# Optimization experiments

Hardware: AMD Instinct MI355X
Metric: run time of the kernel (lower is better)

Reference implementation:

```python
import jax, jax.numpy as jnp
import numpy as np

# ---- Cl(3,0,1) algebra constants (basis blades in bitmask order, bit k = e_k) ----
# metric: e0,e1,e2 square to +1 (p=3), e3 squares to 0 (r=1, the projective/null direction)
_METRIC = [1.0, 1.0, 1.0, 0.0]

def _cayley_table():
    C = np.zeros((16, 16, 16), dtype=np.float32)
    for a in range(16):
        for b in range(16):
            # canonical reordering sign
            s, t = 0, a >> 1
            while t:
                s += bin(t & b).count('1')
                t >>= 1
            val = -1.0 if (s & 1) else 1.0
            for k in range(4):
                if (a >> k) & 1 and (b >> k) & 1:
                    val *= _METRIC[k]
            if val != 0.0:
                C[a, b, a ^ b] += val
    return C

_C = jnp.asarray(_cayley_table())                       # [16,16,16] geometric-product table
_POPC = [bin(i).count('1') for i in range(16)]
_REV = jnp.asarray([(-1.0) ** (g * (g - 1) // 2) for g in _POPC], dtype=jnp.float32)  # reverse signs
_G2 = jnp.asarray([1.0 if g == 2 else 0.0 for g in _POPC], dtype=jnp.float32)         # grade-2 mask
_CENTERS = jnp.arange(10, dtype=jnp.float32)

def _gp(a, b):
    # geometric product for small multivector batches
    return jnp.einsum('...i,...j,ijk->...k', a, b, _C)

def _mv_exp(x, n_terms=16):
    # Taylor-series exponential of a multivector (x is a small [L,16] bivector)
    term = jnp.zeros_like(x).at[..., 0].set(1.0)
    acc = term
    for n in range(1, n_terms):
        term = _gp(term, x) / n
        acc = acc + term
    return acc


def setup_inputs() -> dict:
    key = jax.random.key(0)
    k1, k2, k3, k4 = jax.random.split(key, 4)
    B, N, D, K = 32, 100000, 16, 4
    state = jax.random.normal(k1, (B, N, D), dtype=jnp.float32)
    instruction = jax.random.normal(k2, (B, D), dtype=jnp.float32)
    remap_tables = jnp.eye(10, dtype=jnp.float32)[None].repeat(K, axis=0) \
        + 0.01 * jax.random.normal(k3, (K, 10, 10), dtype=jnp.float32)
    selector_w = jax.random.normal(k4, (K, 2), dtype=jnp.float32) / jnp.sqrt(2.0)
    selector_b = jnp.zeros((K,), dtype=jnp.float32)
    return {"state": state, "instruction": instruction, "remap_tables": remap_tables,
            "selector_w": selector_w, "selector_b": selector_b}


def reference(state, instruction, remap_tables, selector_w, selector_b):
    # ---- PGA motor sandwich product ----
    bv = instruction * _G2                                   # grade-2 projection [L,16]
    M = _mv_exp(-0.5 * bv)                                   # motor [L,16]
    M_rev = M * _REV                                         # reverse(M)
    # Precompute per-row left/right multiplication matrices (avoid [L,N,16,16] outer products)
    Lmat = jnp.einsum('li,ijk->ljk', M, _C)                  # left-mult by M:   x_j -> (M x)_k
    Rmat = jnp.einsum('lj,ijk->lik', M_rev, _C)              # right-mult by ~M: y_i -> (y ~M)_k
    tmp = jnp.einsum('lnj,ljk->lnk', state, Lmat)            # M * state
    spatial = jnp.einsum('lni,lik->lnk', tmp, Rmat)          # (M * state) * ~M   [L,N,16]

    # ---- ColorUnit: soft color remap of grade-0, occupancy into grade-4 ----
    sel_input = jnp.stack([instruction[:, 0], instruction[:, 15]], axis=-1)      # [L,2]
    table_weights = jax.nn.softmax(sel_input @ selector_w.T + selector_b, axis=-1)  # [L,K]
    blended = jnp.einsum('lk,kij->lij', table_weights, remap_tables)             # [L,10,10]
    raw_color = spatial[:, :, 0] * 9.0                                           # [L,N]
    diffs = raw_color[..., None] - _CENTERS                                      # [L,N,10]
    soft_color = jax.nn.softmax(-4.0 * diffs * diffs, axis=-1)                   # [L,N,10]
    remapped = jnp.einsum('lni,lij->lnj', soft_color, blended)                   # [L,N,10]
    new_color = jnp.einsum('lni,i->ln', remapped, _CENTERS) / 9.0
    new_occupancy = 1.0 - remapped[:, :, 0]
    out = spatial.at[:, :, 0].set(new_color).at[:, :, 15].set(new_occupancy)
    return out
```

## Files before the change

kernel.cpp:

```cpp
#include <hip/hip_runtime.h>
#include <math.h>

constexpr int cpopc(int x){ int c=0; while(x){ c += x&1; x >>= 1; } return c; }

constexpr float csign(int a, int b){
    if (a & b & 8) return 0.0f;
    int s = 0;
    for (int t = a >> 1; t; t >>= 1) s += cpopc(t & b);
    return (s & 1) ? -1.0f : 1.0f;
}

__device__ constexpr int EVEN[8] = {0,3,5,6,9,10,12,15};
__device__ constexpr int EIDX[16] = {0,-1,-1,1,-1,2,3,-1,-1,4,5,-1,6,-1,-1,7};
__device__ constexpr float REVE[8] = {1.f,-1.f,-1.f,-1.f,-1.f,-1.f,-1.f,1.f};

#define WS_STRIDE 288

__global__ void setup_kernel(const float* __restrict__ instr,
                             const float* __restrict__ remap,
                             const float* __restrict__ selw,
                             const float* __restrict__ selb,
                             float* __restrict__ ws,
                             int B, int K) {
    const int l = blockIdx.x * blockDim.x + threadIdx.x;
    if (l >= B) return;
    const float* ins = instr + l * 16;

    float bv[8];
    bv[0] = 0.f; bv[7] = 0.f;
    #pragma unroll
    for (int m = 1; m < 7; m++) bv[m] = -0.5f * ins[EVEN[m]];

    float term[8], acc[8];
    #pragma unroll
    for (int m = 0; m < 8; m++){ term[m] = (m==0) ? 1.f : 0.f; acc[m] = term[m]; }
    #pragma unroll
    for (int n = 1; n < 16; n++){
        float nt[8];
        #pragma unroll
        for (int m = 0; m < 8; m++) nt[m] = 0.f;
        #pragma unroll
        for (int ia = 0; ia < 8; ia++){
            #pragma unroll
            for (int ib = 0; ib < 8; ib++){
                const float s = csign(EVEN[ia], EVEN[ib]);
                if (s != 0.f) nt[EIDX[EVEN[ia] ^ EVEN[ib]]] += s * term[ia] * bv[ib];
            }
        }
        const float inv = 1.0f / (float)n;
        #pragma unroll
        for (int m = 0; m < 8; m++){ term[m] = nt[m] * inv; acc[m] += term[m]; }
    }

    float P[64];
    #pragma unroll
    for (int ia = 0; ia < 8; ia++)
        #pragma unroll
        for (int ib = 0; ib < 8; ib++)
            P[ia*8+ib] = acc[ia] * (acc[ib] * REVE[ib]);

    float* o = ws + (size_t)l * WS_STRIDE;
    #pragma unroll
    for (int j = 0; j < 16; j++){
        float Trow[16];
        #pragma unroll
        for (int k = 0; k < 16; k++) Trow[k] = 0.f;
        #pragma unroll
        for (int ia = 0; ia < 8; ia++){
            const int A = EVEN[ia];
            const float sa = csign(A, j);
            if (sa != 0.f){
                #pragma unroll
                for (int ib = 0; ib < 8; ib++){
                    const int Bb = EVEN[ib];
                    const float s = sa * csign(A ^ j, Bb);
                    if (s != 0.f) Trow[j ^ A ^ Bb] += s * P[ia*8+ib];
                }
            }
        }
        #pragma unroll
        for (int k = 0; k < 16; k++) o[j*16 + k] = Trow[k];
    }

    const float s0 = ins[0], s1 = ins[15];
    float w[8];
    float mx = -1e30f;
    for (int k = 0; k < K; k++){
        w[k] = s0 * selw[2*k] + s1 * selw[2*k+1] + selb[k];
        mx = fmaxf(mx, w[k]);
    }
    float Z = 0.f;
    for (int k = 0; k < K; k++){ w[k] = __expf(w[k] - mx); Z += w[k]; }
    const float rZ = 1.f / Z;
    for (int k = 0; k < K; k++) w[k] *= rZ;

    for (int i = 0; i < 10; i++){
        float a1 = 0.f, a2 = 0.f;
        for (int k = 0; k < K; k++){
            const float* rk = remap + (size_t)(k*10 + i) * 10;
            float rd = 0.f;
            #pragma unroll
            for (int j = 0; j < 10; j++) rd += rk[j] * (float)j;
            a1 += w[k] * rd;
            a2 += w[k] * rk[0];
        }
        o[256 + 2*i]     = a1 * (1.f / 9.f);
        o[256 + 2*i + 1] = a2;
    }
}

#define TPB 256
#define EPT 4

__global__ __launch_bounds__(TPB) void apply_kernel(
    const float* __restrict__ state, const float* __restrict__ ws,
    float* __restrict__ out, int N) {
    const int l = blockIdx.y;
    __shared__ float4 sT[64];
    __shared__ float2 svc[10];
    const float* wsl = ws + (size_t)l * WS_STRIDE;
    {
        const int t = threadIdx.x;
        if (t < 64) sT[t] = reinterpret_cast<const float4*>(wsl)[t];
        if (t >= 64 && t < 74) svc[t-64] = reinterpret_cast<const float2*>(wsl + 256)[t-64];
    }
    __syncthreads();

    const int tid    = blockIdx.x * TPB + threadIdx.x;
    const int stride = gridDim.x * TPB;
    const float4* __restrict__ sp = reinterpret_cast<const float4*>(state) + (size_t)l * N * 4;
    float4*       __restrict__ op = reinterpret_cast<float4*>(out)        + (size_t)l * N * 4;

    int nn[EPT];
    float x[EPT][16];
    #pragma unroll
    for (int e = 0; e < EPT; e++){
        nn[e] = tid + e * stride;
        if (nn[e] < N){
            #pragma unroll
            for (int c = 0; c < 4; c++){
                const float4 v = sp[(size_t)nn[e]*4 + c];
                x[e][4*c+0] = v.x; x[e][4*c+1] = v.y; x[e][4*c+2] = v.z; x[e][4*c+3] = v.w;
            }
        } else {
            #pragma unroll
            for (int k = 0; k < 16; k++) x[e][k] = 0.f;
        }
    }

    float y[EPT][16];
    #pragma unroll
    for (int e = 0; e < EPT; e++)
        #pragma unroll
        for (int k = 0; k < 16; k++) y[e][k] = 0.f;

    #pragma unroll
    for (int j = 0; j < 16; j++){
        const float4 t0 = sT[4*j+0], t1 = sT[4*j+1], t2 = sT[4*j+2], t3 = sT[4*j+3];
        #pragma unroll
        for (int e = 0; e < EPT; e++){
            const float xv = x[e][j];
            y[e][0]  += xv * t0.x; y[e][1]  += xv * t0.y; y[e][2]  += xv * t0.z; y[e][3]  += xv * t0.w;
            y[e][4]  += xv * t1.x; y[e][5]  += xv * t1.y; y[e][6]  += xv * t1.z; y[e][7]  += xv * t1.w;
            y[e][8]  += xv * t2.x; y[e][9]  += xv * t2.y; y[e][10] += xv * t2.z; y[e][11] += xv * t2.w;
            y[e][12] += xv * t3.x; y[e][13] += xv * t3.y; y[e][14] += xv * t3.z; y[e][15] += xv * t3.w;
        }
    }

    #pragma unroll
    for (int e = 0; e < EPT; e++){
        const float raw  = y[e][0] * 9.f;
        const float nc   = fminf(fmaxf(rintf(raw), 0.f), 9.f);
        const float dmin = raw - nc;
        const float mlog = -4.f * dmin * dmin;
        float Z = 0.f, c1 = 0.f, c2 = 0.f;
        #pragma unroll
        for (int i = 0; i < 10; i++){
            const float d  = raw - (float)i;
            const float ev = __expf(-4.f*d*d - mlog);
            const float2 v = svc[i];
            Z += ev; c1 += ev * v.x; c2 += ev * v.y;
        }
        const float rZ = 1.f / Z;
        y[e][0]  = c1 * rZ;
        y[e][15] = 1.f - c2 * rZ;
    }

    #pragma unroll
    for (int e = 0; e < EPT; e++){
        if (nn[e] < N){
            #pragma unroll
            for (int c = 0; c < 4; c++)
                op[(size_t)nn[e]*4 + c] = make_float4(y[e][4*c], y[e][4*c+1], y[e][4*c+2], y[e][4*c+3]);
        }
    }
}

extern "C" void kernel_launch(void* const* d_in, const int* in_sizes, int n_in,
                              void* d_out, int out_size, void* d_ws, size_t ws_size,
                              hipStream_t stream) {
    const float* state = (const float*)d_in[0];
    const float* instr = (const float*)d_in[1];
    const float* remap = (const float*)d_in[2];
    const float* selw  = (const float*)d_in[3];
    const float* selb  = (const float*)d_in[4];
    float* ws  = (float*)d_ws;
    float* out = (float*)d_out;

    const int B = in_sizes[1] / 16;
    const int N = in_sizes[0] / (16 * B);
    const int K = in_sizes[4];

    setup_kernel<<<dim3((B + 63) / 64), 64, 0, stream>>>(instr, remap, selw, selb, ws, B, K);

    const int groups = (N + TPB * EPT - 1) / (TPB * EPT);
    apply_kernel<<<dim3(groups, B), TPB, 0, stream>>>(state, ws, out, N);
}
```

Measured before the change: 464.6 us.

## Exploit grade-preserving sandwich structure with block-diagonal transform and nontemporal stores

```diff
diff --git a/kernel.cpp b/kernel.cpp
--- a/kernel.cpp
+++ b/kernel.cpp
@@ -14,7 +14,9 @@
 __device__ constexpr int EIDX[16] = {0,-1,-1,1,-1,2,3,-1,-1,4,5,-1,6,-1,-1,7};
 __device__ constexpr float REVE[8] = {1.f,-1.f,-1.f,-1.f,-1.f,-1.f,-1.f,1.f};
 
-#define WS_STRIDE 288
+typedef float vf4 __attribute__((ext_vector_type(4)));
+
+#define WS_STRIDE 112
 
 __global__ void setup_kernel(const float* __restrict__ instr,
                              const float* __restrict__ remap,
@@ -61,7 +63,7 @@
 
     float* o = ws + (size_t)l * WS_STRIDE;
     #pragma unroll
-    for (int j = 0; j < 16; j++){
+    for (int j = 0; j < 15; j++){
         float Trow[16];
         #pragma unroll
         for (int k = 0; k < 16; k++) Trow[k] = 0.f;
@@ -78,8 +80,24 @@
                 }
             }
         }
-        #pragma unroll
-        for (int k = 0; k < 16; k++) o[j*16 + k] = Trow[k];
+        if (j == 0){
+            o[80] = Trow[0];
+        } else {
+            const int g = cpopc(j);
+            if (g == 1){
+                const int r = (j==1)?0:((j==2)?1:((j==4)?2:3));
+                o[4*r+0]=Trow[1]; o[4*r+1]=Trow[2]; o[4*r+2]=Trow[4]; o[4*r+3]=Trow[8];
+            } else if (g == 2){
+                const int r = (j==3)?0:((j==5)?1:((j==6)?2:((j==9)?3:((j==10)?4:5))));
+                float* p = o + 16 + 8*r;
+                p[0]=Trow[3]; p[1]=Trow[5];  p[2]=Trow[6];  p[3]=Trow[9];
+                p[4]=Trow[10]; p[5]=Trow[12]; p[6]=0.f; p[7]=0.f;
+            } else {
+                const int r = (j==7)?0:((j==11)?1:((j==13)?2:3));
+                float* p = o + 64 + 4*r;
+                p[0]=Trow[7]; p[1]=Trow[11]; p[2]=Trow[13]; p[3]=Trow[14];
+            }
+        }
     }
 
     const float s0 = ins[0], s1 = ins[15];
@@ -104,26 +122,110 @@
             a1 += w[k] * rd;
             a2 += w[k] * rk[0];
         }
-        o[256 + 2*i]     = a1 * (1.f / 9.f);
-        o[256 + 2*i + 1] = a2;
+        o[84 + 2*i]     = a1 * (1.f / 9.f);
+        o[84 + 2*i + 1] = a2;
     }
 }
 
 #define TPB 256
-#define EPT 4
-
-__global__ __launch_bounds__(TPB) void apply_kernel(
+#define EPT 2
+
+__device__ __forceinline__ void transform_one(
+    const float* sW,
+    const float4 a0, const float4 a1, const float4 a2, const float4 a3,
+    float4& o0, float4& o1, float4& o2, float4& o3)
+{
+
+    const float4 g10 = *reinterpret_cast<const float4*>(sW + 0);
+    const float4 g11 = *reinterpret_cast<const float4*>(sW + 4);
+    const float4 g12 = *reinterpret_cast<const float4*>(sW + 8);
+    const float4 g13 = *reinterpret_cast<const float4*>(sW + 12);
+    const float y1 = a0.y*g10.x + a0.z*g11.x + a1.x*g12.x + a2.x*g13.x;
+    const float y2 = a0.y*g10.y + a0.z*g11.y + a1.x*g12.y + a2.x*g13.y;
+    const float y4 = a0.y*g10.z + a0.z*g11.z + a1.x*g12.z + a2.x*g13.z;
+    const float y8 = a0.y*g10.w + a0.z*g11.w + a1.x*g12.w + a2.x*g13.w;
+
+    float y3, y5, y6, y9, y10, y12;
+    {
+        const float4 ra = *reinterpret_cast<const float4*>(sW + 16);
+        const float2 rb = *reinterpret_cast<const float2*>(sW + 20);
+        y3  = a0.w*ra.x; y5  = a0.w*ra.y; y6  = a0.w*ra.z; y9 = a0.w*ra.w;
+        y10 = a0.w*rb.x; y12 = a0.w*rb.y;
+    }
+    {
+        const float4 ra = *reinterpret_cast<const float4*>(sW + 24);
+        const float2 rb = *reinterpret_cast<const float2*>(sW + 28);
+        y3  += a1.y*ra.x; y5  += a1.y*ra.y; y6  += a1.y*ra.z; y9 += a1.y*ra.w;
+        y10 += a1.y*rb.x; y12 += a1.y*rb.y;
+    }
+    {
+        const float4 ra = *reinterpret_cast<const float4*>(sW + 32);
+        const float2 rb = *reinterpret_cast<const float2*>(sW + 36);
+        y3  += a1.z*ra.x; y5  += a1.z*ra.y; y6  += a1.z*ra.z; y9 += a1.z*ra.w;
+        y10 += a1.z*rb.x; y12 += a1.z*rb.y;
+    }
+    {
+        const float4 ra = *reinterpret_cast<const float4*>(sW + 40);
+        const float2 rb = *reinterpret_cast<const float2*>(sW + 44);
+        y3  += a2.y*ra.x; y5  += a2.y*ra.y; y6  += a2.y*ra.z; y9 += a2.y*ra.w;
+        y10 += a2.y*rb.x; y12 += a2.y*rb.y;
+    }
+    {
+        const float4 ra = *reinterpret_cast<const float4*>(sW + 48);
+        const float2 rb = *reinterpret_cast<const float2*>(sW + 52);
+        y3  += a2.z*ra.x; y5  += a2.z*ra.y; y6  += a2.z*ra.z; y9 += a2.z*ra.w;
+        y10 += a2.z*rb.x; y12 += a2.z*rb.y;
+    }
+    {
+        const float4 ra = *reinterpret_cast<const float4*>(sW + 56);
+        const float2 rb = *reinterpret_cast<const float2*>(sW + 60);
+        y3  += a3.x*ra.x; y5  += a3.x*ra.y; y6  += a3.x*ra.z; y9 += a3.x*ra.w;
+        y10 += a3.x*rb.x; y12 += a3.x*rb.y;
+    }
+
+    const float4 g30 = *reinterpret_cast<const float4*>(sW + 64);
+    const float4 g31 = *reinterpret_cast<const float4*>(sW + 68);
+    const float4 g32 = *reinterpret_cast<const float4*>(sW + 72);
+    const float4 g33 = *reinterpret_cast<const float4*>(sW + 76);
+    const float y7  = a1.w*g30.x + a2.w*g31.x + a3.y*g32.x + a3.z*g33.x;
+    const float y11 = a1.w*g30.y + a2.w*g31.y + a3.y*g32.y + a3.z*g33.y;
+    const float y13 = a1.w*g30.z + a2.w*g31.z + a3.y*g32.z + a3.z*g33.z;
+    const float y14 = a1.w*g30.w + a2.w*g31.w + a3.y*g32.w + a3.z*g33.w;
+
+    const float raw  = (sW[80] * a0.x) * 9.f;
+    const float ncf  = fminf(fmaxf(rintf(raw), 0.f), 9.f);
+    const float dmin = raw - ncf;
+    const float mlog = -4.f * dmin * dmin;
+    float Z = 0.f, c1 = 0.f, c2 = 0.f;
+    #pragma unroll
+    for (int i = 0; i < 10; i++){
+        const float d  = raw - (float)i;
+        const float ev = __expf(-4.f*d*d - mlog);
+        const float2 v = reinterpret_cast<const float2*>(sW + 84)[i];
+        Z += ev; c1 += ev * v.x; c2 += ev * v.y;
+    }
+    const float rZ = 1.f / Z;
+
+    o0 = make_float4(c1 * rZ, y1,  y2,  y3);
+    o1 = make_float4(y4,      y5,  y6,  y7);
+    o2 = make_float4(y8,      y9,  y10, y11);
+    o3 = make_float4(y12,     y13, y14, 1.f - c2 * rZ);
+}
+
+__device__ __forceinline__ void nt_store4(float4* p, const float4& v){
+    __builtin_nontemporal_store(*reinterpret_cast<const vf4*>(&v),
+                                reinterpret_cast<vf4*>(p));
+}
+
+__global__ __launch_bounds__(TPB, 4) void apply_kernel(
     const float* __restrict__ state, const float* __restrict__ ws,
-    float* __restrict__ out, int N) {
+    float* __restrict__ out, int N)
+{
     const int l = blockIdx.y;
-    __shared__ float4 sT[64];
-    __shared__ float2 svc[10];
-    const float* wsl = ws + (size_t)l * WS_STRIDE;
-    {
-        const int t = threadIdx.x;
-        if (t < 64) sT[t] = reinterpret_cast<const float4*>(wsl)[t];
-        if (t >= 64 && t < 74) svc[t-64] = reinterpret_cast<const float2*>(wsl + 256)[t-64];
-    }
+    __shared__ float sW[WS_STRIDE];
+    if (threadIdx.x < WS_STRIDE/4)
+        reinterpret_cast<float4*>(sW)[threadIdx.x] =
+            reinterpret_cast<const float4*>(ws + (size_t)l * WS_STRIDE)[threadIdx.x];
     __syncthreads();
 
     const int tid    = blockIdx.x * TPB + threadIdx.x;
@@ -131,68 +233,38 @@
     const float4* __restrict__ sp = reinterpret_cast<const float4*>(state) + (size_t)l * N * 4;
     float4*       __restrict__ op = reinterpret_cast<float4*>(out)        + (size_t)l * N * 4;
 
-    int nn[EPT];
-    float x[EPT][16];
-    #pragma unroll
-    for (int e = 0; e < EPT; e++){
-        nn[e] = tid + e * stride;
-        if (nn[e] < N){
-            #pragma unroll
-            for (int c = 0; c < 4; c++){
-                const float4 v = sp[(size_t)nn[e]*4 + c];
-                x[e][4*c+0] = v.x; x[e][4*c+1] = v.y; x[e][4*c+2] = v.z; x[e][4*c+3] = v.w;
-            }
-        } else {
-            #pragma unroll
-            for (int k = 0; k < 16; k++) x[e][k] = 0.f;
-        }
-    }
-
-    float y[EPT][16];
-    #pragma unroll
-    for (int e = 0; e < EPT; e++)
-        #pragma unroll
-        for (int k = 0; k < 16; k++) y[e][k] = 0.f;
-
-    #pragma unroll
-    for (int j = 0; j < 16; j++){
-        const float4 t0 = sT[4*j+0], t1 = sT[4*j+1], t2 = sT[4*j+2], t3 = sT[4*j+3];
-        #pragma unroll
-        for (int e = 0; e < EPT; e++){
-            const float xv = x[e][j];
-            y[e][0]  += xv * t0.x; y[e][1]  += xv * t0.y; y[e][2]  += xv * t0.z; y[e][3]  += xv * t0.w;
-            y[e][4]  += xv * t1.x; y[e][5]  += xv * t1.y; y[e][6]  += xv * t1.z; y[e][7]  += xv * t1.w;
-            y[e][8]  += xv * t2.x; y[e][9]  += xv * t2.y; y[e][10] += xv * t2.z; y[e][11] += xv * t2.w;
-            y[e][12] += xv * t3.x; y[e][13] += xv * t3.y; y[e][14] += xv * t3.z; y[e][15] += xv * t3.w;
-        }
-    }
-
-    #pragma unroll
-    for (int e = 0; e < EPT; e++){
-        const float raw  = y[e][0] * 9.f;
-        const float nc   = fminf(fmaxf(rintf(raw), 0.f), 9.f);
-        const float dmin = raw - nc;
-        const float mlog = -4.f * dmin * dmin;
-        float Z = 0.f, c1 = 0.f, c2 = 0.f;
-        #pragma unroll
-        for (int i = 0; i < 10; i++){
-            const float d  = raw - (float)i;
-            const float ev = __expf(-4.f*d*d - mlog);
-            const float2 v = svc[i];
-            Z += ev; c1 += ev * v.x; c2 += ev * v.y;
-        }
-        const float rZ = 1.f / Z;
-        y[e][0]  = c1 * rZ;
-        y[e][15] = 1.f - c2 * rZ;
-    }
-
-    #pragma unroll
-    for (int e = 0; e < EPT; e++){
-        if (nn[e] < N){
-            #pragma unroll
-            for (int c = 0; c < 4; c++)
-                op[(size_t)nn[e]*4 + c] = make_float4(y[e][4*c], y[e][4*c+1], y[e][4*c+2], y[e][4*c+3]);
-        }
+    const int n0 = tid;
+    const int n1 = tid + stride;
+    const bool v0 = n0 < N;
+    const bool v1 = n1 < N;
+
+    float4 a0,a1,a2,a3, b0,b1,b2,b3;
+    if (v0){
+        const float4* p = sp + (size_t)n0 * 4;
+        a0 = p[0]; a1 = p[1]; a2 = p[2]; a3 = p[3];
+    } else {
+        a0 = a1 = a2 = a3 = make_float4(0.f,0.f,0.f,0.f);
+    }
+    if (v1){
+        const float4* p = sp + (size_t)n1 * 4;
+        b0 = p[0]; b1 = p[1]; b2 = p[2]; b3 = p[3];
+    } else {
+        b0 = b1 = b2 = b3 = make_float4(0.f,0.f,0.f,0.f);
+    }
+
+    float4 o0,o1,o2,o3, q0,q1,q2,q3;
+    transform_one(sW, a0,a1,a2,a3, o0,o1,o2,o3);
+    transform_one(sW, b0,b1,b2,b3, q0,q1,q2,q3);
+
+    if (v0){
+        float4* p = op + (size_t)n0 * 4;
+        nt_store4(p+0, o0); nt_store4(p+1, o1);
+        nt_store4(p+2, o2); nt_store4(p+3, o3);
+    }
+    if (v1){
+        float4* p = op + (size_t)n1 * 4;
+        nt_store4(p+0, q0); nt_store4(p+1, q1);
+        nt_store4(p+2, q2); nt_store4(p+3, q3);
     }
 }
 
```

Result: slower. 572.0 us (+23.1%).
